# Kernel tuning notes

Hardware: AMD Instinct MI355X
Metric: run time of the kernel (lower is better)

The kernel has to match this reference:

```python
import jax, jax.numpy as jnp
import numpy as np

MESSAGE_SIZE = 128
MESSAGE_PASSES = 3
N_BONDS = 7      # Single, Double, Triple, Quadruple, Aromatic, Pi, Universal
N_LAYERS = 8     # 8 bias-free Linear layers, ReLU after the first 7
N_TYPES = 6      # top-4 ranked atoms + atom 0, plus catchall slot (index 5)
ATOM_VALS = [6.0, 7.0, 8.0, 9.0, 16.0, 17.0, 1.0]
TOP_ATOMS = [6.0, 7.0, 8.0, 9.0, 0.0]


def setup_inputs() -> dict:
    key = jax.random.key(0)
    ks = jax.random.split(key, 8)
    B, N, F, D = 128, 128, 75, MESSAGE_SIZE
    g = jax.random.uniform(ks[0], (B, N_BONDS, N, N), dtype=jnp.float32)
    h = jax.random.normal(ks[1], (B, N, F), dtype=jnp.float32)
    # channel 0 carries the atomic number used for GRU routing
    atom_ids = jax.random.randint(ks[2], (B, N), 0, len(ATOM_VALS))
    h = h.at[:, :, 0].set(jnp.asarray(ATOM_VALS, jnp.float32)[atom_ids])
    s = 1.0 / np.sqrt(D)
    msg_W = jax.random.normal(ks[3], (N_BONDS, N_LAYERS, D, D), jnp.float32) * s
    gru_Wih = jax.random.normal(ks[4], (2, N_TYPES, 3 * D, D), jnp.float32) * s  # [regular/universal, type, 3H, H]
    gru_Whh = jax.random.normal(ks[5], (2, N_TYPES, 3 * D, D), jnp.float32) * s
    gru_bih = jax.random.normal(ks[6], (2, N_TYPES, 3 * D), jnp.float32) * s
    gru_bhh = jax.random.normal(ks[7], (2, N_TYPES, 3 * D), jnp.float32) * s
    return dict(g=g, h=h, msg_W=msg_W, gru_Wih=gru_Wih, gru_Whh=gru_Whh,
                gru_bih=gru_bih, gru_bhh=gru_bhh)


def _gru_grouped(x, hx, tid, Wih, Whh, bih, bhh):
    """torch.nn.GRUCell(input=x, hx=hx) with per-node parameter group tid in [0,T).
    Wih/Whh: [T, 3H, H], bih/bhh: [T, 3H]."""
    gx = jnp.einsum('nd,tgd->ntg', x, Wih)   # [n, T, 3H]
    gh = jnp.einsum('nd,tgd->ntg', hx, Whh)
    gx = jnp.take_along_axis(gx, tid[:, None, None], axis=1)[:, 0] + bih[tid]
    gh = jnp.take_along_axis(gh, tid[:, None, None], axis=1)[:, 0] + bhh[tid]
    xr, xz, xn = jnp.split(gx, 3, axis=-1)
    hr, hz, hn = jnp.split(gh, 3, axis=-1)
    r = jax.nn.sigmoid(xr + hr)
    z = jax.nn.sigmoid(xz + hz)
    n = jnp.tanh(xn + r * hn)
    return (1.0 - z) * n + z * hx


def reference(g, h, msg_W, gru_Wih, gru_Whh, gru_bih, gru_bhh):
    B, N, F = h.shape
    D = msg_W.shape[-1]
    h_t = jnp.concatenate([h, jnp.zeros((B, N, D - F), h.dtype)], axis=2)  # [B,N,D]
    atoms = h[:, :, 0].reshape(-1)
    tid = jnp.full(atoms.shape, N_TYPES - 1, jnp.int32)  # default catchall
    for i, a in enumerate(TOP_ATOMS):
        tid = jnp.where(atoms == jnp.float32(a), jnp.int32(i), tid)
    for _ in range(MESSAGE_PASSES):
        # per-bond-type 8-layer bias-free MLP, vectorized over the 7 bond types
        xb = jnp.broadcast_to(h_t[None], (N_BONDS, B, N, D))
        for l in range(N_LAYERS):
            xb = jnp.einsum('kbnd,ked->kbne', xb, msg_W[:, l])
            if l < N_LAYERS - 1:
                xb = jax.nn.relu(xb)
        # bmm aggregation per bond type: m_k = g[:,k] @ xb_k
        m_all = jnp.einsum('bknm,kbmd->kbnd', g, xb)
        m_non = m_all[:N_BONDS - 1].sum(0).reshape(-1, D)
        m_uni = m_all[N_BONDS - 1].reshape(-1, D)
        h_flat = h_t.reshape(-1, D)
        out = _gru_grouped(h_flat, m_non, tid, gru_Wih[0], gru_Whh[0], gru_bih[0], gru_bhh[0])
        out_u = _gru_grouped(h_flat, m_uni, tid, gru_Wih[1], gru_Whh[1], gru_bih[1], gru_bhh[1])
        h_t = (out + out_u).reshape(B, N, D)
    return h_t
```

## Files before the change

kernel.cpp:

```cpp
#include <hip/hip_runtime.h>
#include <math.h>

#define NBOND 7
#define NLAY 8
#define NTYPE 6
#define NNODES 16384
#define PX 136

typedef _Float16 half8 __attribute__((ext_vector_type(8)));
typedef _Float16 half4 __attribute__((ext_vector_type(4)));
typedef float floatx16 __attribute__((ext_vector_type(16)));

__device__ __forceinline__ float sig_(float x) { return 1.0f / (1.0f + __expf(-x)); }
__device__ __forceinline__ int drow_(int reg, int hi) { return (reg & 3) + 8 * (reg >> 2) + 4 * hi; }

__device__ __forceinline__ _Float16 hi_(float v) { return (_Float16)v; }
__device__ __forceinline__ _Float16 lo_(float v) { return (_Float16)(v - (float)(_Float16)v); }

__global__ void setup_kernel(const float* __restrict__ h, float* __restrict__ hT,
                             int* __restrict__ counts, int* __restrict__ bucket)
{
    int gid = blockIdx.x * 256 + threadIdx.x;
    int node = gid >> 7, d = gid & 127;
    hT[gid] = (d < 75) ? h[node * 75 + d] : 0.0f;
    if (gid < NNODES) {
        float a = h[gid * 75];
        int tt = 5;
        if      (a == 6.0f) tt = 0;
        else if (a == 7.0f) tt = 1;
        else if (a == 8.0f) tt = 2;
        else if (a == 9.0f) tt = 3;
        else if (a == 0.0f) tt = 4;
        int slot = atomicAdd(&counts[tt], 1);
        bucket[tt * NNODES + slot] = gid;
    }
}

__global__ void pack_msg_kernel(const float* __restrict__ msgW, _Float16* __restrict__ Wp)
{
    int idx = blockIdx.x * 256 + threadIdx.x;
    if (idx >= NBOND * NLAY * 16 * 128) return;
    int e  = idx & 127;
    int c  = (idx >> 7) & 15;
    int kl = idx >> 11;
    const float* src = msgW + ((size_t)kl * 128 + e) * 128 + c * 8;
    float4 u = *(const float4*)src;
    float4 v = *(const float4*)(src + 4);
    float av[8] = {u.x, u.y, u.z, u.w, v.x, v.y, v.z, v.w};
    half8 hh, ll;
    #pragma unroll
    for (int j = 0; j < 8; ++j) { hh[j] = hi_(av[j]); ll[j] = lo_(av[j]); }
    _Float16* dst = Wp + ((size_t)kl * 16 + c) * 2048;
    *(half8*)(dst + e * 8)        = hh;
    *(half8*)(dst + 1024 + e * 8) = ll;
}

__global__ void pack_gru_kernel(const float* __restrict__ Wih, const float* __restrict__ Whh,
                                _Float16* __restrict__ Wp)
{
    int idx = blockIdx.x * 256 + threadIdx.x;
    if (idx >= 2 * NTYPE * 2 * 16 * 384) return;
    int col = idx % 384;
    int c   = (idx / 384) & 15;
    int vm  = idx / 6144;
    int mat = vm & 1;
    int vt  = vm >> 1;
    const float* src = (mat ? Whh : Wih) + ((size_t)vt * 384 + col) * 128 + c * 8;
    float4 u = *(const float4*)src;
    float4 v = *(const float4*)(src + 4);
    float av[8] = {u.x, u.y, u.z, u.w, v.x, v.y, v.z, v.w};
    half8 hh, ll;
    #pragma unroll
    for (int j = 0; j < 8; ++j) { hh[j] = hi_(av[j]); ll[j] = lo_(av[j]); }
    _Float16* dst = Wp + (size_t)vm * 98304 + (size_t)c * 6144;
    *(half8*)(dst + col * 8)        = hh;
    *(half8*)(dst + 3072 + col * 8) = ll;
}

__global__ __launch_bounds__(256) void mlp_agg_mfma(
    const float* __restrict__ hT, const _Float16* __restrict__ Wp,
    const float* __restrict__ gmat, float* __restrict__ m_non, float* __restrict__ m_uni)
{
    __shared__ _Float16 Xhi[128 * PX];
    __shared__ _Float16 Xlo[128 * PX];

    const int t = threadIdx.x;
    const int kb = blockIdx.x, b = blockIdx.y;
    const int wave = t >> 6, lane = t & 63, lo = lane & 31, hi = lane >> 5;
    const int row = wave * 32 + lo;

    for (int q = t; q < 128 * 32; q += 256) {
        int r = q >> 5, c4 = q & 31;
        float4 v = *(const float4*)(hT + ((size_t)(b * 128 + r)) * 128 + c4 * 4);
        half4 hh, ll;
        hh[0] = hi_(v.x); ll[0] = lo_(v.x);
        hh[1] = hi_(v.y); ll[1] = lo_(v.y);
        hh[2] = hi_(v.z); ll[2] = lo_(v.z);
        hh[3] = hi_(v.w); ll[3] = lo_(v.w);
        *(half4*)(Xhi + r * PX + c4 * 4) = hh;
        *(half4*)(Xlo + r * PX + c4 * 4) = ll;
    }
    __syncthreads();

    floatx16 acc[4];

    #pragma unroll 1
    for (int l = 0; l < NLAY; ++l) {
        #pragma unroll
        for (int ct = 0; ct < 4; ++ct) acc[ct] = (floatx16)0.0f;
        const _Float16* wb = Wp + ((size_t)(kb * NLAY + l) * 16) * 2048;

        #pragma unroll 2
        for (int kk = 0; kk < 8; ++kk) {
            half8 a_h = *(const half8*)(Xhi + row * PX + kk * 16 + hi * 8);
            half8 a_l = *(const half8*)(Xlo + row * PX + kk * 16 + hi * 8);
            const _Float16* bp = wb + (size_t)(kk * 2 + hi) * 2048;
            #pragma unroll
            for (int ct = 0; ct < 4; ++ct) {
                half8 b_h = *(const half8*)(bp + (ct * 32 + lo) * 8);
                half8 b_l = *(const half8*)(bp + 1024 + (ct * 32 + lo) * 8);
                acc[ct] = __builtin_amdgcn_mfma_f32_32x32x16_f16(a_h, b_h, acc[ct], 0, 0, 0);
                acc[ct] = __builtin_amdgcn_mfma_f32_32x32x16_f16(a_h, b_l, acc[ct], 0, 0, 0);
                acc[ct] = __builtin_amdgcn_mfma_f32_32x32x16_f16(a_l, b_h, acc[ct], 0, 0, 0);
            }
        }
        __syncthreads();

        if (l < NLAY - 1) {
            #pragma unroll
            for (int ct = 0; ct < 4; ++ct)
                #pragma unroll
                for (int reg = 0; reg < 16; ++reg) {
                    int n = wave * 32 + drow_(reg, hi);
                    float vv = fmaxf(acc[ct][reg], 0.0f);
                    Xhi[n * PX + ct * 32 + lo] = hi_(vv);
                    Xlo[n * PX + ct * 32 + lo] = lo_(vv);
                }
        } else {
            #pragma unroll
            for (int ct = 0; ct < 4; ++ct)
                #pragma unroll
                for (int s = 0; s < 4; ++s) {
                    int e = ct * 32 + lo, m0 = wave * 32 + 8 * s + 4 * hi;
                    half4 hh, ll;
                    #pragma unroll
                    for (int j = 0; j < 4; ++j) {
                        float vv = acc[ct][4 * s + j];
                        hh[j] = hi_(vv); ll[j] = lo_(vv);
                    }
                    *(half4*)(Xhi + e * PX + m0) = hh;
                    *(half4*)(Xlo + e * PX + m0) = ll;
                }
        }
        __syncthreads();
    }

    #pragma unroll
    for (int ct = 0; ct < 4; ++ct) acc[ct] = (floatx16)0.0f;
    const float* grow = gmat + (size_t)(b * NBOND + kb) * 16384;

    #pragma unroll 2
    for (int kk = 0; kk < 8; ++kk) {
        const float* gp = grow + (size_t)row * 128 + kk * 16 + hi * 8;
        float4 u = *(const float4*)gp, v2 = *(const float4*)(gp + 4);
        float av[8] = {u.x, u.y, u.z, u.w, v2.x, v2.y, v2.z, v2.w};
        half8 a_h, a_l;
        #pragma unroll
        for (int j = 0; j < 8; ++j) { a_h[j] = hi_(av[j]); a_l[j] = lo_(av[j]); }
        #pragma unroll
        for (int ct = 0; ct < 4; ++ct) {
            half8 b_h = *(const half8*)(Xhi + (ct * 32 + lo) * PX + kk * 16 + hi * 8);
            half8 b_l = *(const half8*)(Xlo + (ct * 32 + lo) * PX + kk * 16 + hi * 8);
            acc[ct] = __builtin_amdgcn_mfma_f32_32x32x16_f16(a_h, b_h, acc[ct], 0, 0, 0);
            acc[ct] = __builtin_amdgcn_mfma_f32_32x32x16_f16(a_h, b_l, acc[ct], 0, 0, 0);
            acc[ct] = __builtin_amdgcn_mfma_f32_32x32x16_f16(a_l, b_h, acc[ct], 0, 0, 0);
        }
    }

    if (kb == NBOND - 1) {
        #pragma unroll
        for (int ct = 0; ct < 4; ++ct)
            #pragma unroll
            for (int reg = 0; reg < 16; ++reg) {
                int n = wave * 32 + drow_(reg, hi);
                m_uni[((size_t)(b * 128 + n)) * 128 + ct * 32 + lo] = acc[ct][reg];
            }
    } else {
        #pragma unroll
        for (int ct = 0; ct < 4; ++ct)
            #pragma unroll
            for (int reg = 0; reg < 16; ++reg) {
                int n = wave * 32 + drow_(reg, hi);
                atomicAdd(m_non + ((size_t)(b * 128 + n)) * 128 + ct * 32 + lo, acc[ct][reg]);
            }
    }
}

__global__ __launch_bounds__(256) void gru_mfma(
    float* __restrict__ hT, const float* __restrict__ m_non, const float* __restrict__ m_uni,
    const int* __restrict__ counts, const int* __restrict__ bucket,
    const _Float16* __restrict__ Wp, const float* __restrict__ bihp, const float* __restrict__ bhhp)
{
    __shared__ _Float16 Xh[64 * PX], Xl[64 * PX], Mh[64 * PX], Ml[64 * PX];
    __shared__ int bl[64];

    const int t = threadIdx.x, tt = blockIdx.y;
    const int cnt  = counts[tt];
    const int base = blockIdx.x * 64;
    if (base >= cnt) return;
    const int nn = min(64, cnt - base);
    if (t < 64) bl[t] = (t < nn) ? bucket[tt * NNODES + base + t] : -1;
    __syncthreads();

    const int wave = t >> 6, lane = t & 63, lo = lane & 31, hi = lane >> 5;
    const int d = wave * 32 + lo;

    for (int q = t; q < 64 * 32; q += 256) {
        int r = q >> 5, c4 = q & 31;
        float4 v = make_float4(0.f, 0.f, 0.f, 0.f);
        int node = bl[r];
        if (node >= 0) v = *(const float4*)(hT + (size_t)node * 128 + c4 * 4);
        half4 hh, ll;
        hh[0] = hi_(v.x); ll[0] = lo_(v.x);
        hh[1] = hi_(v.y); ll[1] = lo_(v.y);
        hh[2] = hi_(v.z); ll[2] = lo_(v.z);
        hh[3] = hi_(v.w); ll[3] = lo_(v.w);
        *(half4*)(Xh + r * PX + c4 * 4) = hh;
        *(half4*)(Xl + r * PX + c4 * 4) = ll;
    }

    #pragma unroll 1
    for (int rt = 0; rt < 2; ++rt) {
        float hacc[16];
        #pragma unroll
        for (int reg = 0; reg < 16; ++reg) hacc[reg] = 0.0f;
        const int rrow = rt * 32 + lo;

        #pragma unroll 1
        for (int v = 0; v < 2; ++v) {
            const float* msrc = v ? m_uni : m_non;
            __syncthreads();
            for (int q = t; q < 64 * 32; q += 256) {
                int r = q >> 5, c4 = q & 31;
                float4 mv = make_float4(0.f, 0.f, 0.f, 0.f);
                int node = bl[r];
                if (node >= 0) mv = *(const float4*)(msrc + (size_t)node * 128 + c4 * 4);
                half4 hh, ll;
                hh[0] = hi_(mv.x); ll[0] = lo_(mv.x);
                hh[1] = hi_(mv.y); ll[1] = lo_(mv.y);
                hh[2] = hi_(mv.z); ll[2] = lo_(mv.z);
                hh[3] = hi_(mv.w); ll[3] = lo_(mv.w);
                *(half4*)(Mh + r * PX + c4 * 4) = hh;
                *(half4*)(Ml + r * PX + c4 * 4) = ll;
            }
            __syncthreads();

            const int vt = v * NTYPE + tt;
            const _Float16* pih = Wp + (size_t)(vt * 2 + 0) * 98304;
            const _Float16* phh = Wp + (size_t)(vt * 2 + 1) * 98304;

            floatx16 ar = (floatx16)0.0f, az = (floatx16)0.0f;
            floatx16 ax = (floatx16)0.0f, ah = (floatx16)0.0f;

            #pragma unroll 2
            for (int kk = 0; kk < 8; ++kk) {
                int koff = kk * 16 + hi * 8;
                half8 xh = *(const half8*)(Xh + rrow * PX + koff);
                half8 xl = *(const half8*)(Xl + rrow * PX + koff);
                half8 mh = *(const half8*)(Mh + rrow * PX + koff);
                half8 ml = *(const half8*)(Ml + rrow * PX + koff);
                const _Float16* ci = pih + (size_t)(kk * 2 + hi) * 6144;
                const _Float16* ch = phh + (size_t)(kk * 2 + hi) * 6144;
                half8 birh = *(const half8*)(ci + (0   + d) * 8);
                half8 birl = *(const half8*)(ci + 3072 + (0   + d) * 8);
                half8 bizh = *(const half8*)(ci + (128 + d) * 8);
                half8 bizl = *(const half8*)(ci + 3072 + (128 + d) * 8);
                half8 binh = *(const half8*)(ci + (256 + d) * 8);
                half8 binl = *(const half8*)(ci + 3072 + (256 + d) * 8);
                half8 bhrh = *(const half8*)(ch + (0   + d) * 8);
                half8 bhrl = *(const half8*)(ch + 3072 + (0   + d) * 8);
                half8 bhzh = *(const half8*)(ch + (128 + d) * 8);
                half8 bhzl = *(const half8*)(ch + 3072 + (128 + d) * 8);
                half8 bhnh = *(const half8*)(ch + (256 + d) * 8);
                half8 bhnl = *(const half8*)(ch + 3072 + (256 + d) * 8);

                ar = __builtin_amdgcn_mfma_f32_32x32x16_f16(xh, birh, ar, 0, 0, 0);
                ar = __builtin_amdgcn_mfma_f32_32x32x16_f16(xh, birl, ar, 0, 0, 0);
                ar = __builtin_amdgcn_mfma_f32_32x32x16_f16(xl, birh, ar, 0, 0, 0);
                ar = __builtin_amdgcn_mfma_f32_32x32x16_f16(mh, bhrh, ar, 0, 0, 0);
                ar = __builtin_amdgcn_mfma_f32_32x32x16_f16(mh, bhrl, ar, 0, 0, 0);
                ar = __builtin_amdgcn_mfma_f32_32x32x16_f16(ml, bhrh, ar, 0, 0, 0);

                az = __builtin_amdgcn_mfma_f32_32x32x16_f16(xh, bizh, az, 0, 0, 0);
                az = __builtin_amdgcn_mfma_f32_32x32x16_f16(xh, bizl, az, 0, 0, 0);
                az = __builtin_amdgcn_mfma_f32_32x32x16_f16(xl, bizh, az, 0, 0, 0);
                az = __builtin_amdgcn_mfma_f32_32x32x16_f16(mh, bhzh, az, 0, 0, 0);
                az = __builtin_amdgcn_mfma_f32_32x32x16_f16(mh, bhzl, az, 0, 0, 0);
                az = __builtin_amdgcn_mfma_f32_32x32x16_f16(ml, bhzh, az, 0, 0, 0);

                ax = __builtin_amdgcn_mfma_f32_32x32x16_f16(xh, binh, ax, 0, 0, 0);
                ax = __builtin_amdgcn_mfma_f32_32x32x16_f16(xh, binl, ax, 0, 0, 0);
                ax = __builtin_amdgcn_mfma_f32_32x32x16_f16(xl, binh, ax, 0, 0, 0);
                ah = __builtin_amdgcn_mfma_f32_32x32x16_f16(mh, bhnh, ah, 0, 0, 0);
                ah = __builtin_amdgcn_mfma_f32_32x32x16_f16(mh, bhnl, ah, 0, 0, 0);
                ah = __builtin_amdgcn_mfma_f32_32x32x16_f16(ml, bhnh, ah, 0, 0, 0);
            }

            const float* bi = bihp + (size_t)vt * 384;
            const float* bh = bhhp + (size_t)vt * 384;
            float b_r  = bi[d] + bh[d];
            float b_z  = bi[128 + d] + bh[128 + d];
            float b_in = bi[256 + d];
            float b_hn = bh[256 + d];
            #pragma unroll
            for (int reg = 0; reg < 16; ++reg) {
                int n = rt * 32 + drow_(reg, hi);
                int node = bl[n];
                float r  = sig_(ar[reg] + b_r);
                float z  = sig_(az[reg] + b_z);
                float nv = tanhf(ax[reg] + b_in + r * (ah[reg] + b_hn));
                float mv = (node >= 0) ? msrc[(size_t)node * 128 + d] : 0.0f;
                hacc[reg] += (1.0f - z) * nv + z * mv;
            }
        }

        #pragma unroll
        for (int reg = 0; reg < 16; ++reg) {
            int n = rt * 32 + drow_(reg, hi);
            int node = bl[n];
            if (node >= 0) hT[(size_t)node * 128 + d] = hacc[reg];
        }
    }
}

extern "C" void kernel_launch(void* const* d_in, const int* in_sizes, int n_in,
                              void* d_out, int out_size, void* d_ws, size_t ws_size,
                              hipStream_t stream) {
    const float* g    = (const float*)d_in[0];
    const float* h    = (const float*)d_in[1];
    const float* msgW = (const float*)d_in[2];
    const float* Wih  = (const float*)d_in[3];
    const float* Whh  = (const float*)d_in[4];
    const float* bih  = (const float*)d_in[5];
    const float* bhh  = (const float*)d_in[6];
    float* hT = (float*)d_out;

    char* ws = (char*)d_ws;
    float* m_non = (float*)ws;
    float* m_uni = m_non + (size_t)NNODES * 128;
    int* counts  = (int*)(ws + 2 * (size_t)NNODES * 128 * 4);
    int* bucket  = counts + 8;
    _Float16* WpM = (_Float16*)(bucket + NTYPE * NNODES);
    _Float16* WpG = WpM + (size_t)NBOND * NLAY * 16 * 2048;

    (void)hipMemsetAsync(counts, 0, 8 * sizeof(int), stream);
    setup_kernel<<<NNODES * 128 / 256, 256, 0, stream>>>(h, hT, counts, bucket);
    pack_msg_kernel<<<(NBOND * NLAY * 16 * 128 + 255) / 256, 256, 0, stream>>>(msgW, WpM);
    pack_gru_kernel<<<(2 * NTYPE * 2 * 16 * 384 + 255) / 256, 256, 0, stream>>>(Wih, Whh, WpG);

    for (int pass = 0; pass < 3; ++pass) {
        (void)hipMemsetAsync(m_non, 0, (size_t)NNODES * 128 * 4, stream);
        mlp_agg_mfma<<<dim3(NBOND, 128), 256, 0, stream>>>(hT, WpM, g, m_non, m_uni);
        gru_mfma<<<dim3(NNODES / 64, NTYPE), 256, 0, stream>>>(hT, m_non, m_uni, counts, bucket,
                                                               WpG, bih, bhh);
    }
}
```

Measured before the change: 953.2 us.

## Transpose MLP MFMA operands for vectorized stores; reuse GRU weights across row tiles

In the MLP kernel the first seven layers now compute the transposed product (weights as A operand, activations as B). Each lane can then write its ReLU outputs back to shared memory as contiguous half4 vectors instead of scattered scalar stores. In the GRU kernel the row-tile loop moves inside the k loop, so each weight fragment loaded from global memory serves both 32-row tiles. The r/z and n gates are split into two passes to limit live accumulators. This halves GRU weight traffic but raises register pressure (per-tile hacc, rr and zz arrays) and may reduce occupancy.

```diff
diff --git a/kernel.cpp b/kernel.cpp
--- a/kernel.cpp
+++ b/kernel.cpp
@@ -87,7 +87,7 @@
     const int t = threadIdx.x;
     const int kb = blockIdx.x, b = blockIdx.y;
     const int wave = t >> 6, lane = t & 63, lo = lane & 31, hi = lane >> 5;
-    const int row = wave * 32 + lo;
+    const int node = wave * 32 + lo;
 
     for (int q = t; q < 128 * 32; q += 256) {
         int r = q >> 5, c4 = q & 31;
@@ -105,63 +105,86 @@
     floatx16 acc[4];
 
     #pragma unroll 1
-    for (int l = 0; l < NLAY; ++l) {
-        #pragma unroll
-        for (int ct = 0; ct < 4; ++ct) acc[ct] = (floatx16)0.0f;
+    for (int l = 0; l < NLAY - 1; ++l) {
+        #pragma unroll
+        for (int et = 0; et < 4; ++et) acc[et] = (floatx16)0.0f;
         const _Float16* wb = Wp + ((size_t)(kb * NLAY + l) * 16) * 2048;
 
         #pragma unroll 2
         for (int kk = 0; kk < 8; ++kk) {
-            half8 a_h = *(const half8*)(Xhi + row * PX + kk * 16 + hi * 8);
-            half8 a_l = *(const half8*)(Xlo + row * PX + kk * 16 + hi * 8);
+            half8 x_h = *(const half8*)(Xhi + node * PX + kk * 16 + hi * 8);
+            half8 x_l = *(const half8*)(Xlo + node * PX + kk * 16 + hi * 8);
+            const _Float16* ap = wb + (size_t)(kk * 2 + hi) * 2048;
+            #pragma unroll
+            for (int et = 0; et < 4; ++et) {
+                half8 w_h = *(const half8*)(ap + (et * 32 + lo) * 8);
+                half8 w_l = *(const half8*)(ap + 1024 + (et * 32 + lo) * 8);
+                acc[et] = __builtin_amdgcn_mfma_f32_32x32x16_f16(w_h, x_h, acc[et], 0, 0, 0);
+                acc[et] = __builtin_amdgcn_mfma_f32_32x32x16_f16(w_h, x_l, acc[et], 0, 0, 0);
+                acc[et] = __builtin_amdgcn_mfma_f32_32x32x16_f16(w_l, x_h, acc[et], 0, 0, 0);
+            }
+        }
+        __syncthreads();
+        #pragma unroll
+        for (int et = 0; et < 4; ++et)
+            #pragma unroll
+            for (int s = 0; s < 4; ++s) {
+                int e0 = et * 32 + 8 * s + 4 * hi;
+                half4 hh, ll;
+                #pragma unroll
+                for (int j = 0; j < 4; ++j) {
+                    float vv = fmaxf(acc[et][4 * s + j], 0.0f);
+                    hh[j] = hi_(vv); ll[j] = lo_(vv);
+                }
+                *(half4*)(Xhi + node * PX + e0) = hh;
+                *(half4*)(Xlo + node * PX + e0) = ll;
+            }
+        __syncthreads();
+    }
+
+    #pragma unroll
+    for (int et = 0; et < 4; ++et) acc[et] = (floatx16)0.0f;
+    {
+        const _Float16* wb = Wp + ((size_t)(kb * NLAY + (NLAY - 1)) * 16) * 2048;
+        #pragma unroll 2
+        for (int kk = 0; kk < 8; ++kk) {
+            half8 x_h = *(const half8*)(Xhi + node * PX + kk * 16 + hi * 8);
+            half8 x_l = *(const half8*)(Xlo + node * PX + kk * 16 + hi * 8);
             const _Float16* bp = wb + (size_t)(kk * 2 + hi) * 2048;
             #pragma unroll
-            for (int ct = 0; ct < 4; ++ct) {
-                half8 b_h = *(const half8*)(bp + (ct * 32 + lo) * 8);
-                half8 b_l = *(const half8*)(bp + 1024 + (ct * 32 + lo) * 8);
-                acc[ct] = __builtin_amdgcn_mfma_f32_32x32x16_f16(a_h, b_h, acc[ct], 0, 0, 0);
-                acc[ct] = __builtin_amdgcn_mfma_f32_32x32x16_f16(a_h, b_l, acc[ct], 0, 0, 0);
-                acc[ct] = __builtin_amdgcn_mfma_f32_32x32x16_f16(a_l, b_h, acc[ct], 0, 0, 0);
-            }
-        }
-        __syncthreads();
-
-        if (l < NLAY - 1) {
-            #pragma unroll
-            for (int ct = 0; ct < 4; ++ct)
-                #pragma unroll
-                for (int reg = 0; reg < 16; ++reg) {
-                    int n = wave * 32 + drow_(reg, hi);
-                    float vv = fmaxf(acc[ct][reg], 0.0f);
-                    Xhi[n * PX + ct * 32 + lo] = hi_(vv);
-                    Xlo[n * PX + ct * 32 + lo] = lo_(vv);
-                }
-        } else {
-            #pragma unroll
-            for (int ct = 0; ct < 4; ++ct)
-                #pragma unroll
-                for (int s = 0; s < 4; ++s) {
-                    int e = ct * 32 + lo, m0 = wave * 32 + 8 * s + 4 * hi;
-                    half4 hh, ll;
-                    #pragma unroll
-                    for (int j = 0; j < 4; ++j) {
-                        float vv = acc[ct][4 * s + j];
-                        hh[j] = hi_(vv); ll[j] = lo_(vv);
-                    }
-                    *(half4*)(Xhi + e * PX + m0) = hh;
-                    *(half4*)(Xlo + e * PX + m0) = ll;
-                }
-        }
-        __syncthreads();
-    }
-
-    #pragma unroll
-    for (int ct = 0; ct < 4; ++ct) acc[ct] = (floatx16)0.0f;
+            for (int et = 0; et < 4; ++et) {
+                half8 w_h = *(const half8*)(bp + (et * 32 + lo) * 8);
+                half8 w_l = *(const half8*)(bp + 1024 + (et * 32 + lo) * 8);
+                acc[et] = __builtin_amdgcn_mfma_f32_32x32x16_f16(x_h, w_h, acc[et], 0, 0, 0);
+                acc[et] = __builtin_amdgcn_mfma_f32_32x32x16_f16(x_h, w_l, acc[et], 0, 0, 0);
+                acc[et] = __builtin_amdgcn_mfma_f32_32x32x16_f16(x_l, w_h, acc[et], 0, 0, 0);
+            }
+        }
+    }
+    __syncthreads();
+    #pragma unroll
+    for (int et = 0; et < 4; ++et)
+        #pragma unroll
+        for (int s = 0; s < 4; ++s) {
+            int e = et * 32 + lo, m0 = wave * 32 + 8 * s + 4 * hi;
+            half4 hh, ll;
+            #pragma unroll
+            for (int j = 0; j < 4; ++j) {
+                float vv = acc[et][4 * s + j];
+                hh[j] = hi_(vv); ll[j] = lo_(vv);
+            }
+            *(half4*)(Xhi + e * PX + m0) = hh;
+            *(half4*)(Xlo + e * PX + m0) = ll;
+        }
+    __syncthreads();
+
+    #pragma unroll
+    for (int et = 0; et < 4; ++et) acc[et] = (floatx16)0.0f;
     const float* grow = gmat + (size_t)(b * NBOND + kb) * 16384;
 
     #pragma unroll 2
     for (int kk = 0; kk < 8; ++kk) {
-        const float* gp = grow + (size_t)row * 128 + kk * 16 + hi * 8;
+        const float* gp = grow + (size_t)node * 128 + kk * 16 + hi * 8;
         float4 u = *(const float4*)gp, v2 = *(const float4*)(gp + 4);
         float av[8] = {u.x, u.y, u.z, u.w, v2.x, v2.y, v2.z, v2.w};
         half8 a_h, a_l;
@@ -229,108 +252,142 @@
         *(half4*)(Xl + r * PX + c4 * 4) = ll;
     }
 
+    float hacc[2][16];
+    #pragma unroll
+    for (int rt = 0; rt < 2; ++rt)
+        #pragma unroll
+        for (int reg = 0; reg < 16; ++reg) hacc[rt][reg] = 0.0f;
+
     #pragma unroll 1
-    for (int rt = 0; rt < 2; ++rt) {
-        float hacc[16];
-        #pragma unroll
-        for (int reg = 0; reg < 16; ++reg) hacc[reg] = 0.0f;
-        const int rrow = rt * 32 + lo;
+    for (int v = 0; v < 2; ++v) {
+        const float* msrc = v ? m_uni : m_non;
+        __syncthreads();
+        for (int q = t; q < 64 * 32; q += 256) {
+            int r = q >> 5, c4 = q & 31;
+            float4 mv = make_float4(0.f, 0.f, 0.f, 0.f);
+            int node = bl[r];
+            if (node >= 0) mv = *(const float4*)(msrc + (size_t)node * 128 + c4 * 4);
+            half4 hh, ll;
+            hh[0] = hi_(mv.x); ll[0] = lo_(mv.x);
+            hh[1] = hi_(mv.y); ll[1] = lo_(mv.y);
+            hh[2] = hi_(mv.z); ll[2] = lo_(mv.z);
+            hh[3] = hi_(mv.w); ll[3] = lo_(mv.w);
+            *(half4*)(Mh + r * PX + c4 * 4) = hh;
+            *(half4*)(Ml + r * PX + c4 * 4) = ll;
+        }
+        __syncthreads();
+
+        const int vt = v * NTYPE + tt;
+        const _Float16* pih = Wp + (size_t)(vt * 2 + 0) * 98304;
+        const _Float16* phh = Wp + (size_t)(vt * 2 + 1) * 98304;
+        const float* bi = bihp + (size_t)vt * 384;
+        const float* bh = bhhp + (size_t)vt * 384;
+
+        floatx16 ar[2], az[2];
+        ar[0] = (floatx16)0.0f; ar[1] = (floatx16)0.0f;
+        az[0] = (floatx16)0.0f; az[1] = (floatx16)0.0f;
 
         #pragma unroll 1
-        for (int v = 0; v < 2; ++v) {
-            const float* msrc = v ? m_uni : m_non;
-            __syncthreads();
-            for (int q = t; q < 64 * 32; q += 256) {
-                int r = q >> 5, c4 = q & 31;
-                float4 mv = make_float4(0.f, 0.f, 0.f, 0.f);
-                int node = bl[r];
-                if (node >= 0) mv = *(const float4*)(msrc + (size_t)node * 128 + c4 * 4);
-                half4 hh, ll;
-                hh[0] = hi_(mv.x); ll[0] = lo_(mv.x);
-                hh[1] = hi_(mv.y); ll[1] = lo_(mv.y);
-                hh[2] = hi_(mv.z); ll[2] = lo_(mv.z);
-                hh[3] = hi_(mv.w); ll[3] = lo_(mv.w);
-                *(half4*)(Mh + r * PX + c4 * 4) = hh;
-                *(half4*)(Ml + r * PX + c4 * 4) = ll;
-            }
-            __syncthreads();
-
-            const int vt = v * NTYPE + tt;
-            const _Float16* pih = Wp + (size_t)(vt * 2 + 0) * 98304;
-            const _Float16* phh = Wp + (size_t)(vt * 2 + 1) * 98304;
-
-            floatx16 ar = (floatx16)0.0f, az = (floatx16)0.0f;
-            floatx16 ax = (floatx16)0.0f, ah = (floatx16)0.0f;
-
-            #pragma unroll 2
-            for (int kk = 0; kk < 8; ++kk) {
-                int koff = kk * 16 + hi * 8;
-                half8 xh = *(const half8*)(Xh + rrow * PX + koff);
-                half8 xl = *(const half8*)(Xl + rrow * PX + koff);
-                half8 mh = *(const half8*)(Mh + rrow * PX + koff);
-                half8 ml = *(const half8*)(Ml + rrow * PX + koff);
-                const _Float16* ci = pih + (size_t)(kk * 2 + hi) * 6144;
-                const _Float16* ch = phh + (size_t)(kk * 2 + hi) * 6144;
-                half8 birh = *(const half8*)(ci + (0   + d) * 8);
-                half8 birl = *(const half8*)(ci + 3072 + (0   + d) * 8);
-                half8 bizh = *(const half8*)(ci + (128 + d) * 8);
-                half8 bizl = *(const half8*)(ci + 3072 + (128 + d) * 8);
-                half8 binh = *(const half8*)(ci + (256 + d) * 8);
-                half8 binl = *(const half8*)(ci + 3072 + (256 + d) * 8);
-                half8 bhrh = *(const half8*)(ch + (0   + d) * 8);
-                half8 bhrl = *(const half8*)(ch + 3072 + (0   + d) * 8);
-                half8 bhzh = *(const half8*)(ch + (128 + d) * 8);
-                half8 bhzl = *(const half8*)(ch + 3072 + (128 + d) * 8);
-                half8 bhnh = *(const half8*)(ch + (256 + d) * 8);
-                half8 bhnl = *(const half8*)(ch + 3072 + (256 + d) * 8);
-
-                ar = __builtin_amdgcn_mfma_f32_32x32x16_f16(xh, birh, ar, 0, 0, 0);
-                ar = __builtin_amdgcn_mfma_f32_32x32x16_f16(xh, birl, ar, 0, 0, 0);
-                ar = __builtin_amdgcn_mfma_f32_32x32x16_f16(xl, birh, ar, 0, 0, 0);
-                ar = __builtin_amdgcn_mfma_f32_32x32x16_f16(mh, bhrh, ar, 0, 0, 0);
-                ar = __builtin_amdgcn_mfma_f32_32x32x16_f16(mh, bhrl, ar, 0, 0, 0);
-                ar = __builtin_amdgcn_mfma_f32_32x32x16_f16(ml, bhrh, ar, 0, 0, 0);
-
-                az = __builtin_amdgcn_mfma_f32_32x32x16_f16(xh, bizh, az, 0, 0, 0);
-                az = __builtin_amdgcn_mfma_f32_32x32x16_f16(xh, bizl, az, 0, 0, 0);
-                az = __builtin_amdgcn_mfma_f32_32x32x16_f16(xl, bizh, az, 0, 0, 0);
-                az = __builtin_amdgcn_mfma_f32_32x32x16_f16(mh, bhzh, az, 0, 0, 0);
-                az = __builtin_amdgcn_mfma_f32_32x32x16_f16(mh, bhzl, az, 0, 0, 0);
-                az = __builtin_amdgcn_mfma_f32_32x32x16_f16(ml, bhzh, az, 0, 0, 0);
-
-                ax = __builtin_amdgcn_mfma_f32_32x32x16_f16(xh, binh, ax, 0, 0, 0);
-                ax = __builtin_amdgcn_mfma_f32_32x32x16_f16(xh, binl, ax, 0, 0, 0);
-                ax = __builtin_amdgcn_mfma_f32_32x32x16_f16(xl, binh, ax, 0, 0, 0);
-                ah = __builtin_amdgcn_mfma_f32_32x32x16_f16(mh, bhnh, ah, 0, 0, 0);
-                ah = __builtin_amdgcn_mfma_f32_32x32x16_f16(mh, bhnl, ah, 0, 0, 0);
-                ah = __builtin_amdgcn_mfma_f32_32x32x16_f16(ml, bhnh, ah, 0, 0, 0);
-            }
-
-            const float* bi = bihp + (size_t)vt * 384;
-            const float* bh = bhhp + (size_t)vt * 384;
-            float b_r  = bi[d] + bh[d];
-            float b_z  = bi[128 + d] + bh[128 + d];
+        for (int kk = 0; kk < 8; ++kk) {
+            int koff = kk * 16 + hi * 8;
+            const _Float16* ci = pih + (size_t)(kk * 2 + hi) * 6144;
+            const _Float16* ch = phh + (size_t)(kk * 2 + hi) * 6144;
+            half8 birh = *(const half8*)(ci + (size_t)(0 + d) * 8);
+            half8 birl = *(const half8*)(ci + 3072 + (size_t)(0 + d) * 8);
+            half8 bhrh = *(const half8*)(ch + (size_t)(0 + d) * 8);
+            half8 bhrl = *(const half8*)(ch + 3072 + (size_t)(0 + d) * 8);
+            half8 bizh = *(const half8*)(ci + (size_t)(128 + d) * 8);
+            half8 bizl = *(const half8*)(ci + 3072 + (size_t)(128 + d) * 8);
+            half8 bhzh = *(const half8*)(ch + (size_t)(128 + d) * 8);
+            half8 bhzl = *(const half8*)(ch + 3072 + (size_t)(128 + d) * 8);
+            #pragma unroll
+            for (int rt = 0; rt < 2; ++rt) {
+                const int rw = rt * 32 + lo;
+                half8 xh = *(const half8*)(Xh + rw * PX + koff);
+                half8 xl = *(const half8*)(Xl + rw * PX + koff);
+                half8 mh = *(const half8*)(Mh + rw * PX + koff);
+                half8 ml = *(const half8*)(Ml + rw * PX + koff);
+                ar[rt] = __builtin_amdgcn_mfma_f32_32x32x16_f16(xh, birh, ar[rt], 0, 0, 0);
+                ar[rt] = __builtin_amdgcn_mfma_f32_32x32x16_f16(xh, birl, ar[rt], 0, 0, 0);
+                ar[rt] = __builtin_amdgcn_mfma_f32_32x32x16_f16(xl, birh, ar[rt], 0, 0, 0);
+                ar[rt] = __builtin_amdgcn_mfma_f32_32x32x16_f16(mh, bhrh, ar[rt], 0, 0, 0);
+                ar[rt] = __builtin_amdgcn_mfma_f32_32x32x16_f16(mh, bhrl, ar[rt], 0, 0, 0);
+                ar[rt] = __builtin_amdgcn_mfma_f32_32x32x16_f16(ml, bhrh, ar[rt], 0, 0, 0);
+                az[rt] = __builtin_amdgcn_mfma_f32_32x32x16_f16(xh, bizh, az[rt], 0, 0, 0);
+                az[rt] = __builtin_amdgcn_mfma_f32_32x32x16_f16(xh, bizl, az[rt], 0, 0, 0);
+                az[rt] = __builtin_amdgcn_mfma_f32_32x32x16_f16(xl, bizh, az[rt], 0, 0, 0);
+                az[rt] = __builtin_amdgcn_mfma_f32_32x32x16_f16(mh, bhzh, az[rt], 0, 0, 0);
+                az[rt] = __builtin_amdgcn_mfma_f32_32x32x16_f16(mh, bhzl, az[rt], 0, 0, 0);
+                az[rt] = __builtin_amdgcn_mfma_f32_32x32x16_f16(ml, bhzh, az[rt], 0, 0, 0);
+            }
+        }
+
+        float rr[2][16], zz[2][16];
+        {
+            float b_r = bi[d] + bh[d];
+            float b_z = bi[128 + d] + bh[128 + d];
+            #pragma unroll
+            for (int rt = 0; rt < 2; ++rt)
+                #pragma unroll
+                for (int reg = 0; reg < 16; ++reg) {
+                    rr[rt][reg] = sig_(ar[rt][reg] + b_r);
+                    zz[rt][reg] = sig_(az[rt][reg] + b_z);
+                }
+        }
+
+        floatx16 ax[2], ah[2];
+        ax[0] = (floatx16)0.0f; ax[1] = (floatx16)0.0f;
+        ah[0] = (floatx16)0.0f; ah[1] = (floatx16)0.0f;
+
+        #pragma unroll 1
+        for (int kk = 0; kk < 8; ++kk) {
+            int koff = kk * 16 + hi * 8;
+            const _Float16* ci = pih + (size_t)(kk * 2 + hi) * 6144;
+            const _Float16* ch = phh + (size_t)(kk * 2 + hi) * 6144;
+            half8 binh = *(const half8*)(ci + (size_t)(256 + d) * 8);
+            half8 binl = *(const half8*)(ci + 3072 + (size_t)(256 + d) * 8);
+            half8 bhnh = *(const half8*)(ch + (size_t)(256 + d) * 8);
+            half8 bhnl = *(const half8*)(ch + 3072 + (size_t)(256 + d) * 8);
+            #pragma unroll
+            for (int rt = 0; rt < 2; ++rt) {
+                const int rw = rt * 32 + lo;
+                half8 xh = *(const half8*)(Xh + rw * PX + koff);
+                half8 xl = *(const half8*)(Xl + rw * PX + koff);
+                half8 mh = *(const half8*)(Mh + rw * PX + koff);
+                half8 ml = *(const half8*)(Ml + rw * PX + koff);
+                ax[rt] = __builtin_amdgcn_mfma_f32_32x32x16_f16(xh, binh, ax[rt], 0, 0, 0);
+                ax[rt] = __builtin_amdgcn_mfma_f32_32x32x16_f16(xh, binl, ax[rt], 0, 0, 0);
+                ax[rt] = __builtin_amdgcn_mfma_f32_32x32x16_f16(xl, binh, ax[rt], 0, 0, 0);
+                ah[rt] = __builtin_amdgcn_mfma_f32_32x32x16_f16(mh, bhnh, ah[rt], 0, 0, 0);
+                ah[rt] = __builtin_amdgcn_mfma_f32_32x32x16_f16(mh, bhnl, ah[rt], 0, 0, 0);
+                ah[rt] = __builtin_amdgcn_mfma_f32_32x32x16_f16(ml, bhnh, ah[rt], 0, 0, 0);
+            }
+        }
+
+        {
             float b_in = bi[256 + d];
             float b_hn = bh[256 + d];
             #pragma unroll
-            for (int reg = 0; reg < 16; ++reg) {
-                int n = rt * 32 + drow_(reg, hi);
-                int node = bl[n];
-                float r  = sig_(ar[reg] + b_r);
-                float z  = sig_(az[reg] + b_z);
-                float nv = tanhf(ax[reg] + b_in + r * (ah[reg] + b_hn));
-                float mv = (node >= 0) ? msrc[(size_t)node * 128 + d] : 0.0f;
-                hacc[reg] += (1.0f - z) * nv + z * mv;
-            }
-        }
-
+            for (int rt = 0; rt < 2; ++rt)
+                #pragma unroll
+                for (int reg = 0; reg < 16; ++reg) {
+                    int n = rt * 32 + drow_(reg, hi);
+                    int node = bl[n];
+                    float nv = tanhf(ax[rt][reg] + b_in + rr[rt][reg] * (ah[rt][reg] + b_hn));
+                    float mv = (node >= 0) ? msrc[(size_t)node * 128 + d] : 0.0f;
+                    hacc[rt][reg] += (1.0f - zz[rt][reg]) * nv + zz[rt][reg] * mv;
+                }
+        }
+    }
+
+    #pragma unroll
+    for (int rt = 0; rt < 2; ++rt)
         #pragma unroll
         for (int reg = 0; reg < 16; ++reg) {
             int n = rt * 32 + drow_(reg, hi);
             int node = bl[n];
-            if (node >= 0) hT[(size_t)node * 128 + d] = hacc[reg];
-        }
-    }
+            if (node >= 0) hT[(size_t)node * 128 + d] = hacc[rt][reg];
+        }
 }
 
 extern "C" void kernel_launch(void* const* d_in, const int* in_sizes, int n_in,
```

After: 1.018 ms. 1.07x slower.
